# Kernel tuning notes

Hardware: AMD Instinct MI355X
Metric: run time of the kernel (lower is better)

Reference implementation:

```python
import jax, jax.numpy as jnp
import numpy as np

B, S, K, N = 4, 2048, 4096, 4096
QMAX = 127.0  # symmetric int8 range used by protoquant qntz


def setup_inputs() -> dict:
    key = jax.random.key(0)
    k1, k2, k3, k4 = jax.random.split(key, 4)
    inp = jax.random.normal(k1, (B, S, K), dtype=jnp.float32)
    # int8 quantized weight, already transposed to [K, N] as in self.qweight_transposed
    qweight_t = jax.random.randint(k2, (K, N), -127, 128, dtype=jnp.int8)
    # per-output-channel dequant scale (wparams)
    wscale = jax.random.uniform(k3, (N,), dtype=jnp.float32, minval=0.001, maxval=0.02)
    bias = jax.random.normal(k4, (N,), dtype=jnp.float32)
    return {"inp": inp, "qweight_t": qweight_t, "wscale": wscale, "bias": bias}


def reference(inp, qweight_t, wscale, bias):
    Bb, Ss, Kk = inp.shape
    x = inp.reshape(Bb * Ss, Kk)  # [M, K]
    # qntz(inp, is_a=True): dynamic per-row symmetric int8 quantization
    amax = jnp.max(jnp.abs(x), axis=1, keepdims=True)  # [M, 1]
    iscale = amax / QMAX                               # per-row dequant scale
    q = jnp.clip(jnp.round(x / jnp.maximum(iscale, 1e-12)), -QMAX, QMAX).astype(jnp.int8)
    d = jnp.matmul(q, qweight_t, preferred_element_type=jnp.int32)  # [M, N]
    # dqntz: scale rows by activation scale, cols by weight scale, add bias
    out = d.astype(jnp.float32) * iscale * wscale[None, :] + bias[None, :]
    return out.reshape(Bb, Ss, -1)
```

## Files before the change

### kernel.cpp

```cpp
#include <hip/hip_runtime.h>

#define M_DIM 8192
#define N_DIM 4096
#define K_DIM 4096

typedef __attribute__((ext_vector_type(4))) int i32x4;

__device__ __forceinline__ void gload_lds16(const void* g, void* l) {
  __builtin_amdgcn_global_load_lds(
      (const __attribute__((address_space(1))) void*)g,
      (__attribute__((address_space(3))) void*)l, 16, 0, 0);
}

#define MFMA_I8(a, b, c) __builtin_amdgcn_mfma_i32_16x16x64_i8((a), (b), (c), 0, 0, 0)

__global__ __launch_bounds__(256) void prep_fused(const float* __restrict__ x,
                                                  signed char* __restrict__ q,
                                                  float* __restrict__ iscale,
                                                  const int* __restrict__ w,
                                                  signed char* __restrict__ wt) {
  const int t = threadIdx.x;
  if (blockIdx.x < M_DIM) {
    const int row = blockIdx.x;
    const float* xr = x + (size_t)row * K_DIM;
    float4 v[4];
    float vmax = 0.f;
#pragma unroll
    for (int i = 0; i < 4; ++i) {
      v[i] = reinterpret_cast<const float4*>(xr)[t + i * 256];
      vmax = fmaxf(vmax, fmaxf(fmaxf(fabsf(v[i].x), fabsf(v[i].y)),
                               fmaxf(fabsf(v[i].z), fabsf(v[i].w))));
    }
#pragma unroll
    for (int off = 32; off > 0; off >>= 1)
      vmax = fmaxf(vmax, __shfl_xor(vmax, off));
    __shared__ float smax[4];
    if ((t & 63) == 0) smax[t >> 6] = vmax;
    __syncthreads();
    vmax = fmaxf(fmaxf(smax[0], smax[1]), fmaxf(smax[2], smax[3]));
    const float isc = vmax * (1.0f / 127.0f);
    if (t == 0) iscale[row] = isc;
    const float s = fmaxf(isc, 1e-12f);
    unsigned* qrow = reinterpret_cast<unsigned*>(q + (size_t)row * K_DIM);
#pragma unroll
    for (int i = 0; i < 4; ++i) {
      int b0 = (int)rintf(fminf(fmaxf(v[i].x / s, -127.f), 127.f));
      int b1 = (int)rintf(fminf(fmaxf(v[i].y / s, -127.f), 127.f));
      int b2 = (int)rintf(fminf(fmaxf(v[i].z / s, -127.f), 127.f));
      int b3 = (int)rintf(fminf(fmaxf(v[i].w / s, -127.f), 127.f));
      qrow[t + i * 256] = (unsigned)(b0 & 0xff) | ((unsigned)(b1 & 0xff) << 8) |
                          ((unsigned)(b2 & 0xff) << 16) |
                          ((unsigned)(b3 & 0xff) << 24);
    }
  } else {
    __shared__ signed char tile[64][68];
    const int lin = blockIdx.x - M_DIM;
    const int n0 = (lin & 63) * 64;
    const int k0 = (lin >> 6) * 64;
#pragma unroll
    for (int i = 0; i < 4; ++i) {
      int idx = t + i * 256;
      int r = idx >> 4;
      int c = idx & 15;
      int4 v = *reinterpret_cast<const int4*>(w + (size_t)(k0 + r) * N_DIM + n0 + c * 4);
      unsigned dw = (unsigned)(v.x & 0xff) | ((unsigned)(v.y & 0xff) << 8) |
                    ((unsigned)(v.z & 0xff) << 16) | ((unsigned)(v.w & 0xff) << 24);
      *reinterpret_cast<unsigned*>(&tile[r][c * 4]) = dw;
    }
    __syncthreads();
#pragma unroll
    for (int i = 0; i < 4; ++i) {
      int idx = t + i * 256;
      int n = idx >> 4;
      int kd = idx & 15;
      unsigned b0 = (unsigned char)tile[kd * 4 + 0][n];
      unsigned b1 = (unsigned char)tile[kd * 4 + 1][n];
      unsigned b2 = (unsigned char)tile[kd * 4 + 2][n];
      unsigned b3 = (unsigned char)tile[kd * 4 + 3][n];
      unsigned dw = b0 | (b1 << 8) | (b2 << 16) | (b3 << 24);
      *reinterpret_cast<unsigned*>(wt + (size_t)(n0 + n) * K_DIM + k0 + kd * 4) = dw;
    }
  }
}

#define BM 256
#define BN 256
#define BK 128
#define NKT (K_DIM / BK)

__global__ __launch_bounds__(512, 2) void gemm_i8(
    const signed char* __restrict__ q,
    const signed char* __restrict__ wt,
    const float* __restrict__ iscale,
    const float* __restrict__ wscale,
    const float* __restrict__ bias,
    float* __restrict__ out)
{
  __shared__ __align__(16) signed char lA[2][BM * BK];
  __shared__ __align__(16) signed char lB[2][BN * BK];

  const int t = threadIdx.x;
  const int l = t & 63;
  const int wid = t >> 6;
  const int wm = wid >> 2;
  const int wn = wid & 3;
  const int fl = l & 15;
  const int fk = l >> 4;
  const int ps0 = fk ^ (fl & 7);
  const int ps1 = (4 + fk) ^ (fl & 7);

  const int lin = blockIdx.y * 16 + blockIdx.x;
  const int swz = (lin & 7) * 64 + (lin >> 3);
  const int m0 = (swz >> 4) * BM;
  const int n0 = (swz & 15) * BN;

  const int srow = t >> 3;
  const int ss = t & 7;
  const unsigned gss = (unsigned)((ss ^ (srow & 7)) << 4);
  const int a0r = srow, a1r = 128 + srow, a2r = 64 + srow, a3r = 192 + srow;
  const int blr = ((srow >> 5) << 6) + (srow & 31);
  const int b0r = blr, b1r = 128 + blr, b2r = 32 + blr, b3r = 160 + blr;

  const unsigned goA0 = (unsigned)(m0 + a0r) * K_DIM + gss;
  const unsigned goA1 = (unsigned)(m0 + a1r) * K_DIM + gss;
  const unsigned goA2 = (unsigned)(m0 + a2r) * K_DIM + gss;
  const unsigned goA3 = (unsigned)(m0 + a3r) * K_DIM + gss;
  const unsigned goB0 = (unsigned)(n0 + b0r) * K_DIM + gss;
  const unsigned goB1 = (unsigned)(n0 + b1r) * K_DIM + gss;
  const unsigned goB2 = (unsigned)(n0 + b2r) * K_DIM + gss;
  const unsigned goB3 = (unsigned)(n0 + b3r) * K_DIM + gss;
  const int loA0 = a0r * BK + (ss << 4), loA1 = a1r * BK + (ss << 4);
  const int loA2 = a2r * BK + (ss << 4), loA3 = a3r * BK + (ss << 4);
  const int loB0 = b0r * BK + (ss << 4), loB1 = b1r * BK + (ss << 4);
  const int loB2 = b2r * BK + (ss << 4), loB3 = b3r * BK + (ss << 4);

  i32x4 acc[8][4] = {};
  i32x4 af[4][2], bf0[2][2], bf1[2][2];

  gload_lds16(q + goA0, &lA[0][0] + loA0);
  gload_lds16(q + goA1, &lA[0][0] + loA1);
  gload_lds16(wt + goB0, &lB[0][0] + loB0);
  gload_lds16(wt + goB1, &lB[0][0] + loB1);
  gload_lds16(wt + goB2, &lB[0][0] + loB2);
  gload_lds16(wt + goB3, &lB[0][0] + loB3);
  gload_lds16(q + goA2, &lA[0][0] + loA2);
  gload_lds16(q + goA3, &lA[0][0] + loA3);
  asm volatile("s_waitcnt vmcnt(4)" ::: "memory");
  __builtin_amdgcn_s_barrier();

  for (int kt = 0; kt < NKT; ++kt) {
    const int cur = kt & 1;
    const signed char* lAc = &lA[cur][0];
    const signed char* lBc = &lB[cur][0];
    signed char* lAn = &lA[cur ^ 1][0];
    signed char* lBn = &lB[cur ^ 1][0];
    const unsigned kbn = (unsigned)(((kt + 1) & (NKT - 1)) * BK);

#pragma unroll
    for (int mi = 0; mi < 4; ++mi) {
      const int row = wm * 128 + mi * 16 + fl;
      af[mi][0] = *(const i32x4*)(lAc + row * BK + ps0 * 16);
      af[mi][1] = *(const i32x4*)(lAc + row * BK + ps1 * 16);
    }
#pragma unroll
    for (int ni = 0; ni < 2; ++ni) {
      const int row = wn * 64 + ni * 16 + fl;
      bf0[ni][0] = *(const i32x4*)(lBc + row * BK + ps0 * 16);
      bf0[ni][1] = *(const i32x4*)(lBc + row * BK + ps1 * 16);
    }
    gload_lds16(q + (goA0 + kbn), lAn + loA0);
    gload_lds16(q + (goA1 + kbn), lAn + loA1);
    asm volatile("s_waitcnt lgkmcnt(0)" ::: "memory");
    __builtin_amdgcn_sched_barrier(0);
    __builtin_amdgcn_s_setprio(1);
#pragma unroll
    for (int mi = 0; mi < 4; ++mi)
#pragma unroll
      for (int ni = 0; ni < 2; ++ni) {
        acc[mi][ni] = MFMA_I8(af[mi][0], bf0[ni][0], acc[mi][ni]);
        acc[mi][ni] = MFMA_I8(af[mi][1], bf0[ni][1], acc[mi][ni]);
      }
    __builtin_amdgcn_s_setprio(0);
    asm volatile("s_waitcnt vmcnt(2)" ::: "memory");
    __builtin_amdgcn_s_barrier();

#pragma unroll
    for (int ni = 0; ni < 2; ++ni) {
      const int row = wn * 64 + 32 + ni * 16 + fl;
      bf1[ni][0] = *(const i32x4*)(lBc + row * BK + ps0 * 16);
      bf1[ni][1] = *(const i32x4*)(lBc + row * BK + ps1 * 16);
    }
    gload_lds16(wt + (goB0 + kbn), lBn + loB0);
    gload_lds16(wt + (goB1 + kbn), lBn + loB1);
    asm volatile("s_waitcnt lgkmcnt(0)" ::: "memory");
    __builtin_amdgcn_sched_barrier(0);
    __builtin_amdgcn_s_setprio(1);
#pragma unroll
    for (int mi = 0; mi < 4; ++mi)
#pragma unroll
      for (int ni = 0; ni < 2; ++ni) {
        acc[mi][2 + ni] = MFMA_I8(af[mi][0], bf1[ni][0], acc[mi][2 + ni]);
        acc[mi][2 + ni] = MFMA_I8(af[mi][1], bf1[ni][1], acc[mi][2 + ni]);
      }
    __builtin_amdgcn_s_setprio(0);

#pragma unroll
    for (int mi = 0; mi < 4; ++mi) {
      const int row = wm * 128 + 64 + mi * 16 + fl;
      af[mi][0] = *(const i32x4*)(lAc + row * BK + ps0 * 16);
      af[mi][1] = *(const i32x4*)(lAc + row * BK + ps1 * 16);
    }
    gload_lds16(wt + (goB2 + kbn), lBn + loB2);
    gload_lds16(wt + (goB3 + kbn), lBn + loB3);
    gload_lds16(q + (goA2 + kbn), lAn + loA2);
    gload_lds16(q + (goA3 + kbn), lAn + loA3);
    asm volatile("s_waitcnt lgkmcnt(0)" ::: "memory");
    __builtin_amdgcn_sched_barrier(0);
    __builtin_amdgcn_s_setprio(1);
#pragma unroll
    for (int mi = 0; mi < 4; ++mi)
#pragma unroll
      for (int ni = 0; ni < 2; ++ni) {
        acc[4 + mi][2 + ni] = MFMA_I8(af[mi][0], bf1[ni][0], acc[4 + mi][2 + ni]);
        acc[4 + mi][2 + ni] = MFMA_I8(af[mi][1], bf1[ni][1], acc[4 + mi][2 + ni]);
      }
#pragma unroll
    for (int mi = 0; mi < 4; ++mi)
#pragma unroll
      for (int ni = 0; ni < 2; ++ni) {
        acc[4 + mi][ni] = MFMA_I8(af[mi][0], bf0[ni][0], acc[4 + mi][ni]);
        acc[4 + mi][ni] = MFMA_I8(af[mi][1], bf0[ni][1], acc[4 + mi][ni]);
      }
    __builtin_amdgcn_s_setprio(0);
    asm volatile("s_waitcnt vmcnt(4)" ::: "memory");
    __builtin_amdgcn_s_barrier();
  }

  const int colb = n0 + wn * 64 + fl;
  const int rowb = m0 + wm * 128 + fk * 4;
#pragma unroll
  for (int mi = 0; mi < 8; ++mi) {
    const int rowoff = ((mi >> 2) * 64 + (mi & 3) * 16);
    float is4[4];
#pragma unroll
    for (int r = 0; r < 4; ++r) is4[r] = iscale[rowb + rowoff + r];
#pragma unroll
    for (int ni = 0; ni < 4; ++ni) {
      const int col = colb + (ni >> 1) * 32 + (ni & 1) * 16;
      const float wsc = wscale[col];
      const float bs = bias[col];
#pragma unroll
      for (int r = 0; r < 4; ++r) {
        out[(size_t)(rowb + rowoff + r) * N_DIM + col] =
            (float)acc[mi][ni][r] * is4[r] * wsc + bs;
      }
    }
  }
}

extern "C" void kernel_launch(void* const* d_in, const int* in_sizes, int n_in,
                              void* d_out, int out_size, void* d_ws, size_t ws_size,
                              hipStream_t stream) {
  const float* inp = (const float*)d_in[0];
  const int* wq32 = (const int*)d_in[1];
  const float* wscale = (const float*)d_in[2];
  const float* bias = (const float*)d_in[3];
  float* out = (float*)d_out;

  signed char* q = (signed char*)d_ws;
  signed char* wt = q + (size_t)M_DIM * K_DIM;
  float* iscale = (float*)(wt + (size_t)N_DIM * K_DIM);

  prep_fused<<<M_DIM + (N_DIM / 64) * (K_DIM / 64), 256, 0, stream>>>(
      inp, q, iscale, wq32, wt);
  gemm_i8<<<dim3(N_DIM / BN, M_DIM / BM), 512, 0, stream>>>(q, wt, iscale, wscale,
                                                            bias, out);
}
```

Baseline: 180.5 us.

## Switch int8 GEMM to 32x32x32 MFMA with k-slab LDS layout

Replaces the 16x16x64 int8 MFMA tiles with 32x32x32 MFMA (i32x16 accumulators) and reorganizes LDS into k-slab-major regions of 16-byte columns, so each global_load_lds lane writes a contiguous chunk without XOR swizzling. The main loop becomes two phases of 16 MFMAs, each loading half the K tile, and the epilogue is remapped to the 32x32 output layout. The aim is fewer LDS reads per MFMA and higher MFMA throughput per instruction. It risks LDS bank conflicts from the unswizzled layout and changes the prefetch wait counts.

```diff
diff --git a/kernel.cpp b/kernel.cpp
--- a/kernel.cpp
+++ b/kernel.cpp
@@ -5,6 +5,7 @@
 #define K_DIM 4096
 
 typedef __attribute__((ext_vector_type(4))) int i32x4;
+typedef __attribute__((ext_vector_type(16))) int i32x16;
 
 __device__ __forceinline__ void gload_lds16(const void* g, void* l) {
   __builtin_amdgcn_global_load_lds(
@@ -12,7 +13,7 @@
       (__attribute__((address_space(3))) void*)l, 16, 0, 0);
 }
 
-#define MFMA_I8(a, b, c) __builtin_amdgcn_mfma_i32_16x16x64_i8((a), (b), (c), 0, 0, 0)
+#define MFMA32(a, b, c) __builtin_amdgcn_mfma_i32_32x32x32_i8((a), (b), (c), 0, 0, 0)
 
 __global__ __launch_bounds__(256) void prep_fused(const float* __restrict__ x,
                                                   signed char* __restrict__ q,
@@ -87,6 +88,7 @@
 #define BN 256
 #define BK 128
 #define NKT (K_DIM / BK)
+#define REG (8 * 256 * 16)
 
 __global__ __launch_bounds__(512, 2) void gemm_i8(
     const signed char* __restrict__ q,
@@ -96,55 +98,39 @@
     const float* __restrict__ bias,
     float* __restrict__ out)
 {
-  __shared__ __align__(16) signed char lA[2][BM * BK];
-  __shared__ __align__(16) signed char lB[2][BN * BK];
+  __shared__ __align__(16) signed char lA[2][REG];
+  __shared__ __align__(16) signed char lB[2][REG];
 
   const int t = threadIdx.x;
   const int l = t & 63;
   const int wid = t >> 6;
   const int wm = wid >> 2;
   const int wn = wid & 3;
-  const int fl = l & 15;
-  const int fk = l >> 4;
-  const int ps0 = fk ^ (fl & 7);
-  const int ps1 = (4 + fk) ^ (fl & 7);
+  const int fl32 = l & 31;
+  const int fh = l >> 5;
 
   const int lin = blockIdx.y * 16 + blockIdx.x;
   const int swz = (lin & 7) * 64 + (lin >> 3);
   const int m0 = (swz >> 4) * BM;
   const int n0 = (swz & 15) * BN;
 
-  const int srow = t >> 3;
-  const int ss = t & 7;
-  const unsigned gss = (unsigned)((ss ^ (srow & 7)) << 4);
-  const int a0r = srow, a1r = 128 + srow, a2r = 64 + srow, a3r = 192 + srow;
-  const int blr = ((srow >> 5) << 6) + (srow & 31);
-  const int b0r = blr, b1r = 128 + blr, b2r = 32 + blr, b3r = 160 + blr;
-
-  const unsigned goA0 = (unsigned)(m0 + a0r) * K_DIM + gss;
-  const unsigned goA1 = (unsigned)(m0 + a1r) * K_DIM + gss;
-  const unsigned goA2 = (unsigned)(m0 + a2r) * K_DIM + gss;
-  const unsigned goA3 = (unsigned)(m0 + a3r) * K_DIM + gss;
-  const unsigned goB0 = (unsigned)(n0 + b0r) * K_DIM + gss;
-  const unsigned goB1 = (unsigned)(n0 + b1r) * K_DIM + gss;
-  const unsigned goB2 = (unsigned)(n0 + b2r) * K_DIM + gss;
-  const unsigned goB3 = (unsigned)(n0 + b3r) * K_DIM + gss;
-  const int loA0 = a0r * BK + (ss << 4), loA1 = a1r * BK + (ss << 4);
-  const int loA2 = a2r * BK + (ss << 4), loA3 = a3r * BK + (ss << 4);
-  const int loB0 = b0r * BK + (ss << 4), loB1 = b1r * BK + (ss << 4);
-  const int loB2 = b2r * BK + (ss << 4), loB3 = b3r * BK + (ss << 4);
-
-  i32x4 acc[8][4] = {};
-  i32x4 af[4][2], bf0[2][2], bf1[2][2];
-
-  gload_lds16(q + goA0, &lA[0][0] + loA0);
-  gload_lds16(q + goA1, &lA[0][0] + loA1);
-  gload_lds16(wt + goB0, &lB[0][0] + loB0);
-  gload_lds16(wt + goB1, &lB[0][0] + loB1);
-  gload_lds16(wt + goB2, &lB[0][0] + loB2);
-  gload_lds16(wt + goB3, &lB[0][0] + loB3);
-  gload_lds16(q + goA2, &lA[0][0] + loA2);
-  gload_lds16(q + goA3, &lA[0][0] + loA3);
+  const int ar = t & 255;
+  const int as_ = t >> 8;
+  const unsigned goA = (unsigned)(m0 + ar) * K_DIM + (unsigned)(as_ << 4);
+  const unsigned goB = (unsigned)(n0 + ar) * K_DIM + (unsigned)(as_ << 4);
+  const int lo = t << 4;
+
+  const int abase = fh * 4096 + (wm * 128 + fl32) * 16;
+  const int bbase = fh * 4096 + (wn * 64 + fl32) * 16;
+
+  i32x16 acc[4][2] = {};
+  i32x4 af[4][2], bf[2][2];
+
+#pragma unroll
+  for (int j = 0; j < 4; ++j) {
+    gload_lds16(q + (goA + j * 32), &lA[0][0] + lo + j * 8192);
+    gload_lds16(wt + (goB + j * 32), &lB[0][0] + lo + j * 8192);
+  }
   asm volatile("s_waitcnt vmcnt(4)" ::: "memory");
   __builtin_amdgcn_s_barrier();
 
@@ -158,101 +144,81 @@
 
 #pragma unroll
     for (int mi = 0; mi < 4; ++mi) {
-      const int row = wm * 128 + mi * 16 + fl;
-      af[mi][0] = *(const i32x4*)(lAc + row * BK + ps0 * 16);
-      af[mi][1] = *(const i32x4*)(lAc + row * BK + ps1 * 16);
+      af[mi][0] = *(const i32x4*)(lAc + abase + mi * 512);
+      af[mi][1] = *(const i32x4*)(lAc + 8192 + abase + mi * 512);
     }
 #pragma unroll
     for (int ni = 0; ni < 2; ++ni) {
-      const int row = wn * 64 + ni * 16 + fl;
-      bf0[ni][0] = *(const i32x4*)(lBc + row * BK + ps0 * 16);
-      bf0[ni][1] = *(const i32x4*)(lBc + row * BK + ps1 * 16);
-    }
-    gload_lds16(q + (goA0 + kbn), lAn + loA0);
-    gload_lds16(q + (goA1 + kbn), lAn + loA1);
+      bf[ni][0] = *(const i32x4*)(lBc + bbase + ni * 512);
+      bf[ni][1] = *(const i32x4*)(lBc + 8192 + bbase + ni * 512);
+    }
+    gload_lds16(q + (goA + kbn), lAn + lo);
+    gload_lds16(wt + (goB + kbn), lBn + lo);
+    gload_lds16(q + (goA + kbn + 32), lAn + lo + 8192);
+    gload_lds16(wt + (goB + kbn + 32), lBn + lo + 8192);
     asm volatile("s_waitcnt lgkmcnt(0)" ::: "memory");
     __builtin_amdgcn_sched_barrier(0);
     __builtin_amdgcn_s_setprio(1);
 #pragma unroll
-    for (int mi = 0; mi < 4; ++mi)
-#pragma unroll
-      for (int ni = 0; ni < 2; ++ni) {
-        acc[mi][ni] = MFMA_I8(af[mi][0], bf0[ni][0], acc[mi][ni]);
-        acc[mi][ni] = MFMA_I8(af[mi][1], bf0[ni][1], acc[mi][ni]);
-      }
+    for (int ks = 0; ks < 2; ++ks)
+#pragma unroll
+      for (int mi = 0; mi < 4; ++mi)
+#pragma unroll
+        for (int ni = 0; ni < 2; ++ni)
+          acc[mi][ni] = MFMA32(af[mi][ks], bf[ni][ks], acc[mi][ni]);
     __builtin_amdgcn_s_setprio(0);
-    asm volatile("s_waitcnt vmcnt(2)" ::: "memory");
+    asm volatile("s_waitcnt vmcnt(4)" ::: "memory");
     __builtin_amdgcn_s_barrier();
 
 #pragma unroll
+    for (int mi = 0; mi < 4; ++mi) {
+      af[mi][0] = *(const i32x4*)(lAc + 16384 + abase + mi * 512);
+      af[mi][1] = *(const i32x4*)(lAc + 24576 + abase + mi * 512);
+    }
+#pragma unroll
     for (int ni = 0; ni < 2; ++ni) {
-      const int row = wn * 64 + 32 + ni * 16 + fl;
-      bf1[ni][0] = *(const i32x4*)(lBc + row * BK + ps0 * 16);
-      bf1[ni][1] = *(const i32x4*)(lBc + row * BK + ps1 * 16);
-    }
-    gload_lds16(wt + (goB0 + kbn), lBn + loB0);
-    gload_lds16(wt + (goB1 + kbn), lBn + loB1);
+      bf[ni][0] = *(const i32x4*)(lBc + 16384 + bbase + ni * 512);
+      bf[ni][1] = *(const i32x4*)(lBc + 24576 + bbase + ni * 512);
+    }
+    gload_lds16(q + (goA + kbn + 64), lAn + lo + 16384);
+    gload_lds16(wt + (goB + kbn + 64), lBn + lo + 16384);
+    gload_lds16(q + (goA + kbn + 96), lAn + lo + 24576);
+    gload_lds16(wt + (goB + kbn + 96), lBn + lo + 24576);
     asm volatile("s_waitcnt lgkmcnt(0)" ::: "memory");
     __builtin_amdgcn_sched_barrier(0);
     __builtin_amdgcn_s_setprio(1);
 #pragma unroll
-    for (int mi = 0; mi < 4; ++mi)
-#pragma unroll
-      for (int ni = 0; ni < 2; ++ni) {
-        acc[mi][2 + ni] = MFMA_I8(af[mi][0], bf1[ni][0], acc[mi][2 + ni]);
-        acc[mi][2 + ni] = MFMA_I8(af[mi][1], bf1[ni][1], acc[mi][2 + ni]);
-      }
-    __builtin_amdgcn_s_setprio(0);
-
-#pragma unroll
-    for (int mi = 0; mi < 4; ++mi) {
-      const int row = wm * 128 + 64 + mi * 16 + fl;
-      af[mi][0] = *(const i32x4*)(lAc + row * BK + ps0 * 16);
-      af[mi][1] = *(const i32x4*)(lAc + row * BK + ps1 * 16);
-    }
-    gload_lds16(wt + (goB2 + kbn), lBn + loB2);
-    gload_lds16(wt + (goB3 + kbn), lBn + loB3);
-    gload_lds16(q + (goA2 + kbn), lAn + loA2);
-    gload_lds16(q + (goA3 + kbn), lAn + loA3);
-    asm volatile("s_waitcnt lgkmcnt(0)" ::: "memory");
-    __builtin_amdgcn_sched_barrier(0);
-    __builtin_amdgcn_s_setprio(1);
-#pragma unroll
-    for (int mi = 0; mi < 4; ++mi)
-#pragma unroll
-      for (int ni = 0; ni < 2; ++ni) {
-        acc[4 + mi][2 + ni] = MFMA_I8(af[mi][0], bf1[ni][0], acc[4 + mi][2 + ni]);
-        acc[4 + mi][2 + ni] = MFMA_I8(af[mi][1], bf1[ni][1], acc[4 + mi][2 + ni]);
-      }
-#pragma unroll
-    for (int mi = 0; mi < 4; ++mi)
-#pragma unroll
-      for (int ni = 0; ni < 2; ++ni) {
-        acc[4 + mi][ni] = MFMA_I8(af[mi][0], bf0[ni][0], acc[4 + mi][ni]);
-        acc[4 + mi][ni] = MFMA_I8(af[mi][1], bf0[ni][1], acc[4 + mi][ni]);
-      }
+    for (int ks = 0; ks < 2; ++ks)
+#pragma unroll
+      for (int mi = 0; mi < 4; ++mi)
+#pragma unroll
+        for (int ni = 0; ni < 2; ++ni)
+          acc[mi][ni] = MFMA32(af[mi][ks], bf[ni][ks], acc[mi][ni]);
     __builtin_amdgcn_s_setprio(0);
     asm volatile("s_waitcnt vmcnt(4)" ::: "memory");
     __builtin_amdgcn_s_barrier();
   }
 
-  const int colb = n0 + wn * 64 + fl;
-  const int rowb = m0 + wm * 128 + fk * 4;
-#pragma unroll
-  for (int mi = 0; mi < 8; ++mi) {
-    const int rowoff = ((mi >> 2) * 64 + (mi & 3) * 16);
-    float is4[4];
-#pragma unroll
-    for (int r = 0; r < 4; ++r) is4[r] = iscale[rowb + rowoff + r];
-#pragma unroll
-    for (int ni = 0; ni < 4; ++ni) {
-      const int col = colb + (ni >> 1) * 32 + (ni & 1) * 16;
-      const float wsc = wscale[col];
-      const float bs = bias[col];
-#pragma unroll
-      for (int r = 0; r < 4; ++r) {
-        out[(size_t)(rowb + rowoff + r) * N_DIM + col] =
-            (float)acc[mi][ni][r] * is4[r] * wsc + bs;
+  const int colb = n0 + wn * 64 + fl32;
+  const int rowbase = m0 + wm * 128 + fh * 4;
+#pragma unroll
+  for (int mi = 0; mi < 4; ++mi) {
+#pragma unroll
+    for (int rg = 0; rg < 4; ++rg) {
+      const int row0 = rowbase + mi * 32 + rg * 8;
+      float is4[4];
+#pragma unroll
+      for (int r = 0; r < 4; ++r) is4[r] = iscale[row0 + r];
+#pragma unroll
+      for (int nj = 0; nj < 2; ++nj) {
+        const int col = colb + nj * 32;
+        const float wsc = wscale[col];
+        const float bs = bias[col];
+#pragma unroll
+        for (int r = 0; r < 4; ++r) {
+          out[(size_t)(row0 + r) * N_DIM + col] =
+              (float)acc[mi][nj][rg * 4 + r] * is4[r] * wsc + bs;
+        }
       }
     }
   }
```

Measured after the change: 337.7 us. +87.1%, slower.

## Peel last K iteration and interleave epilogue stores with final MFMAs

Applied to the files above, without the earlier changes.

Peels the final K tile out of the main loop, which removes the wasted wrap-around prefetch. In the peeled tile, each quadrant of accumulators is written out as soon as its MFMAs finish, so output stores overlap with the remaining matrix math. The stores also switch to nontemporal. This adds code size and register pressure, and the ordering of stores against MFMAs is up to the compiler.

```diff
diff --git a/kernel.cpp b/kernel.cpp
--- a/kernel.cpp
+++ b/kernel.cpp
@@ -137,6 +137,30 @@
   i32x4 acc[8][4] = {};
   i32x4 af[4][2], bf0[2][2], bf1[2][2];
 
+  const int colb = n0 + wn * 64 + fl;
+  const int rowb = m0 + wm * 128 + fk * 4;
+
+#define STORE_QUAD(mb, nb)                                                   \
+  {                                                                          \
+    _Pragma("unroll") for (int mi = 0; mi < 4; ++mi) {                       \
+      const int rowoff = ((mb) ? 64 : 0) + mi * 16;                          \
+      float is4[4];                                                          \
+      _Pragma("unroll") for (int r = 0; r < 4; ++r) is4[r] =                 \
+          iscale[rowb + rowoff + r];                                         \
+      _Pragma("unroll") for (int nj = 0; nj < 2; ++nj) {                     \
+        const int ni = (nb) + nj;                                            \
+        const int col = colb + (ni >> 1) * 32 + (ni & 1) * 16;               \
+        const float wsc = wscale[col];                                       \
+        const float bs = bias[col];                                          \
+        _Pragma("unroll") for (int r = 0; r < 4; ++r) {                      \
+          float vout = (float)acc[(mb) + mi][ni][r] * is4[r] * wsc + bs;     \
+          __builtin_nontemporal_store(                                       \
+              vout, &out[(size_t)(rowb + rowoff + r) * N_DIM + col]);        \
+        }                                                                    \
+      }                                                                      \
+    }                                                                        \
+  }
+
   gload_lds16(q + goA0, &lA[0][0] + loA0);
   gload_lds16(q + goA1, &lA[0][0] + loA1);
   gload_lds16(wt + goB0, &lB[0][0] + loB0);
@@ -148,13 +172,13 @@
   asm volatile("s_waitcnt vmcnt(4)" ::: "memory");
   __builtin_amdgcn_s_barrier();
 
-  for (int kt = 0; kt < NKT; ++kt) {
+  for (int kt = 0; kt < NKT - 1; ++kt) {
     const int cur = kt & 1;
     const signed char* lAc = &lA[cur][0];
     const signed char* lBc = &lB[cur][0];
     signed char* lAn = &lA[cur ^ 1][0];
     signed char* lBn = &lB[cur ^ 1][0];
-    const unsigned kbn = (unsigned)(((kt + 1) & (NKT - 1)) * BK);
+    const unsigned kbn = (unsigned)((kt + 1) * BK);
 
 #pragma unroll
     for (int mi = 0; mi < 4; ++mi) {
@@ -236,26 +260,79 @@
     __builtin_amdgcn_s_barrier();
   }
 
-  const int colb = n0 + wn * 64 + fl;
-  const int rowb = m0 + wm * 128 + fk * 4;
-#pragma unroll
-  for (int mi = 0; mi < 8; ++mi) {
-    const int rowoff = ((mi >> 2) * 64 + (mi & 3) * 16);
-    float is4[4];
-#pragma unroll
-    for (int r = 0; r < 4; ++r) is4[r] = iscale[rowb + rowoff + r];
-#pragma unroll
-    for (int ni = 0; ni < 4; ++ni) {
-      const int col = colb + (ni >> 1) * 32 + (ni & 1) * 16;
-      const float wsc = wscale[col];
-      const float bs = bias[col];
-#pragma unroll
-      for (int r = 0; r < 4; ++r) {
-        out[(size_t)(rowb + rowoff + r) * N_DIM + col] =
-            (float)acc[mi][ni][r] * is4[r] * wsc + bs;
-      }
-    }
+  asm volatile("s_waitcnt vmcnt(0)" ::: "memory");
+  __builtin_amdgcn_s_barrier();
+
+  {
+    const signed char* lAc = &lA[1][0];
+    const signed char* lBc = &lB[1][0];
+
+#pragma unroll
+    for (int mi = 0; mi < 4; ++mi) {
+      const int row = wm * 128 + mi * 16 + fl;
+      af[mi][0] = *(const i32x4*)(lAc + row * BK + ps0 * 16);
+      af[mi][1] = *(const i32x4*)(lAc + row * BK + ps1 * 16);
+    }
+#pragma unroll
+    for (int ni = 0; ni < 2; ++ni) {
+      const int row = wn * 64 + ni * 16 + fl;
+      bf0[ni][0] = *(const i32x4*)(lBc + row * BK + ps0 * 16);
+      bf0[ni][1] = *(const i32x4*)(lBc + row * BK + ps1 * 16);
+    }
+    asm volatile("s_waitcnt lgkmcnt(0)" ::: "memory");
+    __builtin_amdgcn_sched_barrier(0);
+#pragma unroll
+    for (int mi = 0; mi < 4; ++mi)
+#pragma unroll
+      for (int ni = 0; ni < 2; ++ni) {
+        acc[mi][ni] = MFMA_I8(af[mi][0], bf0[ni][0], acc[mi][ni]);
+        acc[mi][ni] = MFMA_I8(af[mi][1], bf0[ni][1], acc[mi][ni]);
+      }
+    STORE_QUAD(0, 0)
+
+#pragma unroll
+    for (int ni = 0; ni < 2; ++ni) {
+      const int row = wn * 64 + 32 + ni * 16 + fl;
+      bf1[ni][0] = *(const i32x4*)(lBc + row * BK + ps0 * 16);
+      bf1[ni][1] = *(const i32x4*)(lBc + row * BK + ps1 * 16);
+    }
+    asm volatile("s_waitcnt lgkmcnt(0)" ::: "memory");
+    __builtin_amdgcn_sched_barrier(0);
+#pragma unroll
+    for (int mi = 0; mi < 4; ++mi)
+#pragma unroll
+      for (int ni = 0; ni < 2; ++ni) {
+        acc[mi][2 + ni] = MFMA_I8(af[mi][0], bf1[ni][0], acc[mi][2 + ni]);
+        acc[mi][2 + ni] = MFMA_I8(af[mi][1], bf1[ni][1], acc[mi][2 + ni]);
+      }
+    STORE_QUAD(0, 2)
+
+#pragma unroll
+    for (int mi = 0; mi < 4; ++mi) {
+      const int row = wm * 128 + 64 + mi * 16 + fl;
+      af[mi][0] = *(const i32x4*)(lAc + row * BK + ps0 * 16);
+      af[mi][1] = *(const i32x4*)(lAc + row * BK + ps1 * 16);
+    }
+    asm volatile("s_waitcnt lgkmcnt(0)" ::: "memory");
+    __builtin_amdgcn_sched_barrier(0);
+#pragma unroll
+    for (int mi = 0; mi < 4; ++mi)
+#pragma unroll
+      for (int ni = 0; ni < 2; ++ni) {
+        acc[4 + mi][2 + ni] = MFMA_I8(af[mi][0], bf1[ni][0], acc[4 + mi][2 + ni]);
+        acc[4 + mi][2 + ni] = MFMA_I8(af[mi][1], bf1[ni][1], acc[4 + mi][2 + ni]);
+      }
+    STORE_QUAD(4, 2)
+#pragma unroll
+    for (int mi = 0; mi < 4; ++mi)
+#pragma unroll
+      for (int ni = 0; ni < 2; ++ni) {
+        acc[4 + mi][ni] = MFMA_I8(af[mi][0], bf0[ni][0], acc[4 + mi][ni]);
+        acc[4 + mi][ni] = MFMA_I8(af[mi][1], bf0[ni][1], acc[4 + mi][ni]);
+      }
+    STORE_QUAD(4, 0)
   }
+#undef STORE_QUAD
 }
 
 extern "C" void kernel_launch(void* const* d_in, const int* in_sizes, int n_in,
```

Measured after the change: 172.6 us. 1.05x faster.
